# Kernel optimization log

Hardware: AMD Instinct MI355X
Metric: run time of the kernel (lower is better)

## Reference

```python
import jax, jax.numpy as jnp
import numpy as np

B, NH, NPTS = 16, 64, 2048
NEIGHS = 20   # knn neighbors in EdgeConv
K_SEL = 512   # topk points selected
EPS = 1e-5    # BatchNorm eps


def setup_inputs() -> dict:
    key = jax.random.key(0)
    ks = jax.random.split(key, 8)
    xyz = jax.random.normal(ks[0], (B, 3, NPTS), jnp.float32)
    seq1 = jax.random.normal(ks[1], (B, NH, NPTS), jnp.float32)
    perm = jax.random.permutation(ks[2], NPTS)
    # fc: Conv1d(n_h,n_h,1) + BN1d (eval-mode stats)
    W_fc = jax.random.normal(ks[3], (NH, NH), jnp.float32) * 0.1
    b_fc = jnp.zeros((NH,), jnp.float32)
    bn1_gamma = jnp.ones((NH,), jnp.float32)
    bn1_beta = jnp.zeros((NH,), jnp.float32)
    bn1_mean = jnp.zeros((NH,), jnp.float32)
    bn1_var = jnp.ones((NH,), jnp.float32)
    # EdgeConv: Conv2d(2*n_h, n_h, 1, bias=False) + BN2d
    W_ec = jax.random.normal(ks[4], (NH, 2 * NH), jnp.float32) * 0.05
    bn2_gamma = jnp.ones((NH,), jnp.float32)
    bn2_beta = jnp.zeros((NH,), jnp.float32)
    bn2_mean = jnp.zeros((NH,), jnp.float32)
    bn2_var = jnp.ones((NH,), jnp.float32)
    # Discriminator Bilinear(n_h, n_h, 1), xavier-uniform weight, zero bias
    lim = float(np.sqrt(6.0 / (NH + NH)))
    W_b = jax.random.uniform(ks[5], (NH, NH), jnp.float32, -lim, lim)
    b_b = jnp.zeros((), jnp.float32)
    return dict(xyz=xyz, seq1=seq1, perm=perm, W_fc=W_fc, b_fc=b_fc,
                bn1_gamma=bn1_gamma, bn1_beta=bn1_beta, bn1_mean=bn1_mean, bn1_var=bn1_var,
                W_ec=W_ec, bn2_gamma=bn2_gamma, bn2_beta=bn2_beta, bn2_mean=bn2_mean, bn2_var=bn2_var,
                W_b=W_b, b_b=b_b)


def reference(xyz, seq1, perm, W_fc, b_fc, bn1_gamma, bn1_beta, bn1_mean, bn1_var,
              W_ec, bn2_gamma, bn2_beta, bn2_mean, bn2_var, W_b, b_b):
    def fc(x):  # x: [B, NH, N] -> Conv1d(1x1) + BN1d(eval) + ReLU
        y = jnp.einsum('oc,bcn->bon', W_fc, x) + b_fc[None, :, None]
        scale = bn1_gamma / jnp.sqrt(bn1_var + EPS)
        y = (y - bn1_mean[None, :, None]) * scale[None, :, None] + bn1_beta[None, :, None]
        return jax.nn.relu(y)

    seq2 = seq1[:, :, perm]                       # shuffled negative sample
    h1 = fc(seq1)                                 # [B, NH, N]
    h2 = fc(seq2)

    # --- EdgeConv(center): knn in feature space ---
    x2 = jnp.sum(h1 * h1, axis=1)                 # [B, N]
    d = 2.0 * jnp.einsum('bcn,bcm->bnm', h1, h1) - x2[:, :, None] - x2[:, None, :]
    _, nidx = jax.lax.top_k(d, NEIGHS)            # [B, N, K] nearest neighbors

    pts = jnp.transpose(h1, (0, 2, 1))            # [B, N, NH]
    nb = jax.vmap(lambda p, i: p[i])(pts, nidx)   # [B, N, K, NH] gather
    ctr = jnp.broadcast_to(pts[:, :, None, :], nb.shape)
    feat = jnp.concatenate([nb - ctr, ctr], axis=-1)   # [B, N, K, 2*NH]

    y = jnp.einsum('bnkc,oc->bnko', feat, W_ec)   # 1x1 conv
    scale2 = bn2_gamma / jnp.sqrt(bn2_var + EPS)
    y = (y - bn2_mean) * scale2 + bn2_beta        # BN2d over channel (last axis)
    y = jnp.where(y >= 0, y, 0.2 * y)             # LeakyReLU(0.2)
    hn1 = jnp.max(y, axis=2)                      # max over k -> [B, N, NH]

    X = jax.nn.sigmoid(hn1)                       # summary per point, [B, N, NH]

    # --- Discriminator: Bilinear(n_h, n_h, 1) ---
    h1t = pts                                     # [B, N, NH]
    h2t = jnp.transpose(h2, (0, 2, 1))
    sc1 = jnp.einsum('bnc,cd,bnd->bn', h1t, W_b, X) + b_b
    sc2 = jnp.einsum('bnc,cd,bnd->bn', h2t, W_b, X) + b_b
    ret = jnp.concatenate([sc1, sc2], axis=1)     # [B, 2N]

    scores = jax.nn.sigmoid(sc1)                  # ret[:, :N]
    values, idx = jax.lax.top_k(scores, K_SEL)    # [B, K_SEL]

    gi = idx[:, None, :]
    seq_static = jnp.take_along_axis(seq1, jnp.broadcast_to(gi, (B, NH, K_SEL)), axis=2)
    seq = seq_static * values[:, None, :]
    xyz_static = jnp.take_along_axis(xyz, jnp.broadcast_to(gi, (B, 3, K_SEL)), axis=2)
    xyz_out = xyz_static * values[:, None, :]
    return seq, values, idx, ret, xyz_static, xyz_out
```

## Files before the change

kernel.cpp:

```cpp
#include <hip/hip_runtime.h>
#include <math.h>

#define NB 16
#define NH 64
#define NPTS 2048
#define NEIGHS 20
#define KSEL 512
#define EPSV 1e-5f
#define NINF -3.0e38f

#define OFF_SEQ 0
#define OFF_VAL (NB*NH*KSEL)
#define OFF_IDX (OFF_VAL + NB*KSEL)
#define OFF_RET (OFF_IDX + NB*KSEL)
#define OFF_XST (OFF_RET + NB*2*NPTS)
#define OFF_XO  (OFF_XST + NB*3*KSEL)

__device__ __forceinline__ bool better(float av, int ai, float bv, int bi) {
  return (av > bv) || (av == bv && ai < bi);
}

__global__ __launch_bounds__(256) void k_fc(const float* __restrict__ seq1,
                                            const float* __restrict__ Wfc,
                                            const float* __restrict__ bfc,
                                            const float* __restrict__ b1g,
                                            const float* __restrict__ b1b,
                                            const float* __restrict__ b1m,
                                            const float* __restrict__ b1v,
                                            const float* __restrict__ Wec,
                                            float* __restrict__ pts,
                                            float* __restrict__ ptsT,
                                            float* __restrict__ G1,
                                            float* __restrict__ G2,
                                            float* __restrict__ x2) {
  const int b = blockIdx.y, n0 = blockIdx.x * 64;
  const int tid = threadIdx.x, l = tid & 63, w = tid >> 6;
  const int n = n0 + l;
  __shared__ float ptL[64*65];
  const float* sq = seq1 + (size_t)b*NH*NPTS + n;
  float x[64];
  #pragma unroll
  for (int c = 0; c < 64; ++c) x[c] = sq[(size_t)c*NPTS];

  for (int oo = 0; oo < 16; ++oo) {
    const int o = w*16 + oo;
    float acc = 0.f;
    const float* ar = Wfc + o*64;
    #pragma unroll
    for (int c = 0; c < 64; c += 4) {
      float4 a4 = *(const float4*)(ar + c);
      acc = fmaf(a4.x, x[c],   acc);
      acc = fmaf(a4.y, x[c+1], acc);
      acc = fmaf(a4.z, x[c+2], acc);
      acc = fmaf(a4.w, x[c+3], acc);
    }
    float s1 = b1g[o] / sqrtf(b1v[o] + EPSV);
    float y  = (acc + bfc[o] - b1m[o]) * s1 + b1b[o];
    ptL[l*65 + o] = fmaxf(y, 0.f);
  }
  __syncthreads();
  float pt[64];
  #pragma unroll
  for (int c = 0; c < 64; ++c) pt[c] = ptL[l*65 + c];
  if (w == 0) {
    float s2 = 0.f;
    #pragma unroll
    for (int c = 0; c < 64; ++c) s2 = fmaf(pt[c], pt[c], s2);
    x2[(size_t)b*NPTS + n] = s2;
  }
  const size_t base = ((size_t)b*NPTS + n0)*NH;
  for (int t = w*16; t < w*16 + 16; ++t) pts[base + t*64 + l] = ptL[t*65 + l];
  for (int c = w*16; c < w*16 + 16; ++c)
    ptsT[((size_t)b*NH + c)*NPTS + n] = ptL[l*65 + c];
  __syncthreads();

  for (int oo = 0; oo < 16; ++oo) {
    const int o = w*16 + oo;
    const float* w1 = Wec + o*128;
    float a1 = 0.f;
    #pragma unroll
    for (int c = 0; c < 64; c += 4) {
      float4 u = *(const float4*)(w1 + c);
      a1 = fmaf(u.x, pt[c],   a1); a1 = fmaf(u.y, pt[c+1], a1);
      a1 = fmaf(u.z, pt[c+2], a1); a1 = fmaf(u.w, pt[c+3], a1);
    }
    ptL[l*65 + o] = a1;
  }
  __syncthreads();
  for (int t = w*16; t < w*16 + 16; ++t) G1[base + t*64 + l] = ptL[t*65 + l];
  __syncthreads();

  for (int oo = 0; oo < 16; ++oo) {
    const int o = w*16 + oo;
    const float* w2 = Wec + o*128 + 64;
    float a2 = 0.f;
    #pragma unroll
    for (int c = 0; c < 64; c += 4) {
      float4 v = *(const float4*)(w2 + c);
      a2 = fmaf(v.x, pt[c],   a2); a2 = fmaf(v.y, pt[c+1], a2);
      a2 = fmaf(v.z, pt[c+2], a2); a2 = fmaf(v.w, pt[c+3], a2);
    }
    ptL[l*65 + o] = a2;
  }
  __syncthreads();
  for (int t = w*16; t < w*16 + 16; ++t) G2[base + t*64 + l] = ptL[t*65 + l];
}

#define FMA4(A, s, F) { (A).x = fmaf((s),(F).x,(A).x); (A).y = fmaf((s),(F).y,(A).y); \
                        (A).z = fmaf((s),(F).z,(A).z); (A).w = fmaf((s),(F).w,(A).w); }

#define CAND(KV, CI) { float cv_=(KV); int ci_=(CI); \
  { bool c_=cv_>L0v; float nv_=c_?cv_:L0v; int ni_=c_?ci_:L0i; float ov_=L0v; int oi_=L0i; cv_=c_?ov_:cv_; ci_=c_?oi_:ci_; L0v=nv_; L0i=ni_; } \
  { bool c_=cv_>L1v; float nv_=c_?cv_:L1v; int ni_=c_?ci_:L1i; float ov_=L1v; int oi_=L1i; cv_=c_?ov_:cv_; ci_=c_?oi_:ci_; L1v=nv_; L1i=ni_; } \
  { bool c_=cv_>L2v; float nv_=c_?cv_:L2v; int ni_=c_?ci_:L2i; float ov_=L2v; int oi_=L2i; cv_=c_?ov_:cv_; ci_=c_?oi_:ci_; L2v=nv_; L2i=ni_; } \
  { bool c_=cv_>L3v; float nv_=c_?cv_:L3v; int ni_=c_?ci_:L3i; float ov_=L3v; int oi_=L3i; cv_=c_?ov_:cv_; ci_=c_?oi_:ci_; L3v=nv_; L3i=ni_; } \
  bool bb_=better(cv_,ci_,bv,bi); bv=bb_?cv_:bv; bi=bb_?ci_:bi; }

#define FCAND(JB, AV, XV) { bool av_=((taken_>>(JB))&1u)==0u; float kv_=fmaf(2.f,(AV),-(XV)); \
  int ci_=cbase+((JB)>>2)*256+((JB)&3); bool bt_=av_&&better(kv_,ci_,pv,pi); \
  pv=bt_?kv_:pv; pi=bt_?ci_:pi; pj=bt_?(JB):pj; }

#define SELROW(T0,T1,T2,T3,RI) { \
  float L0v=NINF,L1v=NINF,L2v=NINF,L3v=NINF; \
  int   L0i=0x7fffffff,L1i=0x7fffffff,L2i=0x7fffffff,L3i=0x7fffffff; \
  float bv=NINF; int bi=0x7fffffff; \
  CAND(fmaf(2.f,(T0).x,-x0.x), cbase+0)   CAND(fmaf(2.f,(T0).y,-x0.y), cbase+1) \
  CAND(fmaf(2.f,(T0).z,-x0.z), cbase+2)   CAND(fmaf(2.f,(T0).w,-x0.w), cbase+3) \
  CAND(fmaf(2.f,(T1).x,-x1.x), cbase+256) CAND(fmaf(2.f,(T1).y,-x1.y), cbase+257) \
  CAND(fmaf(2.f,(T1).z,-x1.z), cbase+258) CAND(fmaf(2.f,(T1).w,-x1.w), cbase+259) \
  CAND(fmaf(2.f,(T2).x,-x2q.x), cbase+512) CAND(fmaf(2.f,(T2).y,-x2q.y), cbase+513) \
  CAND(fmaf(2.f,(T2).z,-x2q.z), cbase+514) CAND(fmaf(2.f,(T2).w,-x2q.w), cbase+515) \
  CAND(fmaf(2.f,(T3).x,-x3.x), cbase+768) CAND(fmaf(2.f,(T3).y,-x3.y), cbase+769) \
  CAND(fmaf(2.f,(T3).z,-x3.z), cbase+770) CAND(fmaf(2.f,(T3).w,-x3.w), cbase+771) \
  float h0v=L0v,h1v=L1v,h2v=L2v,h3v=L3v; \
  int   e0_=L0i,e1_=L1i,e2_=L2i,e3_=L3i; \
  float myV_=0.f; int myNb_=0; float lastv_=NINF; int lasti_=0x7fffffff; \
  for (int t20_=0; t20_<NEIGHS; ++t20_) { \
    float gv=h0v; int gi=e0_; \
    for (int m_=32; m_>=1; m_>>=1) { \
      float ov=__shfl_xor(gv,m_,64); int oi=__shfl_xor(gi,m_,64); \
      bool bt=better(ov,oi,gv,gi); gv=bt?ov:gv; gi=bt?oi:gi; } \
    bool win=(h0v==gv)&&(e0_==gi); \
    h0v=win?h1v:h0v; e0_=win?e1_:e0_; h1v=win?h2v:h1v; e1_=win?e2_:e1_; \
    h2v=win?h3v:h2v; e2_=win?e3_:e2_; h3v=win?NINF:h3v; e3_=win?0x7fffffff:e3_; \
    if (l==t20_){myV_=gv;myNb_=gi;} lastv_=gv; lasti_=gi; \
  } \
  bool flag_ = better(bv, bi, lastv_, lasti_); \
  if (__any((int)flag_)) { \
    unsigned taken_ = 0u; \
    for (int t20_=0; t20_<NEIGHS; ++t20_) { \
      float pv=NINF; int pi=0x7fffffff; int pj=0; \
      FCAND(0,(T0).x,x0.x)  FCAND(1,(T0).y,x0.y)  FCAND(2,(T0).z,x0.z)  FCAND(3,(T0).w,x0.w) \
      FCAND(4,(T1).x,x1.x)  FCAND(5,(T1).y,x1.y)  FCAND(6,(T1).z,x1.z)  FCAND(7,(T1).w,x1.w) \
      FCAND(8,(T2).x,x2q.x) FCAND(9,(T2).y,x2q.y) FCAND(10,(T2).z,x2q.z) FCAND(11,(T2).w,x2q.w) \
      FCAND(12,(T3).x,x3.x) FCAND(13,(T3).y,x3.y) FCAND(14,(T3).z,x3.z) FCAND(15,(T3).w,x3.w) \
      float gv=pv; int gi=pi; \
      for (int m_=32; m_>=1; m_>>=1) { \
        float ov=__shfl_xor(gv,m_,64); int oi=__shfl_xor(gi,m_,64); \
        bool bt=better(ov,oi,gv,gi); gv=bt?ov:gv; gi=bt?oi:gi; } \
      if ((pv==gv)&&(pi==gi)) taken_ |= (1u<<pj); \
      if (l==t20_){myV_=gv;myNb_=gi;} \
    } \
  } \
  if (l < NEIGHS) { \
    mrgV[((g*4+(RI))*2+h)*20 + l] = myV_; \
    mrgI[((g*4+(RI))*2+h)*20 + l] = myNb_; \
  } }

__global__ __launch_bounds__(512, 2) void k_knn(const float* __restrict__ pts,
                                                const float* __restrict__ ptsT,
                                                const float* __restrict__ x2,
                                                int* __restrict__ nidx) {
  const int lin = blockIdx.x;
  const int b  = ((lin & 7) << 1) | ((lin >> 3) & 1);
  const int rg = lin >> 4;
  const int tid = threadIdx.x, w = tid >> 6, l = tid & 63;
  const int g = w >> 1, h = w & 1;
  const int r0 = rg*16;

  __shared__ float colB[2][8192];
  __shared__ float rowS[16*64];
  __shared__ float mrgV[16*2*20];
  __shared__ int   mrgI[16*2*20];

  const float* Tb = ptsT + (size_t)b*NH*NPTS;

  if (tid < 256) {
    int rr = tid >> 4, c4 = (tid & 15) * 4;
    *(float4*)&rowS[rr*64 + c4] =
        *(const float4*)(pts + ((size_t)b*NPTS + r0 + rr)*NH + c4);
  }
  #pragma unroll
  for (int s = 0; s < 4; ++s) {
    float4 v = *(const float4*)(Tb + (w*4+s)*256 + l*4);
    *(float4*)&colB[0][(w*4+s)*256 + l*4] = v;
  }
  __syncthreads();

  float4 A00={0,0,0,0},A01={0,0,0,0},A02={0,0,0,0},A03={0,0,0,0};
  float4 A10={0,0,0,0},A11={0,0,0,0},A12={0,0,0,0},A13={0,0,0,0};
  float4 A20={0,0,0,0},A21={0,0,0,0},A22={0,0,0,0},A23={0,0,0,0};
  float4 A30={0,0,0,0},A31={0,0,0,0},A32={0,0,0,0},A33={0,0,0,0};

  #pragma unroll 1
  for (int t = 0; t < 16; ++t) {
    float4 st0, st1, st2, st3;
    if (t < 15) {
      const float* src = Tb + (size_t)(t+1)*8192 + w*1024 + l*4;
      st0 = *(const float4*)(src);
      st1 = *(const float4*)(src + 256);
      st2 = *(const float4*)(src + 512);
      st3 = *(const float4*)(src + 768);
    }
    const float* cb = &colB[t & 1][h*1024 + l*4];
    const float* rs = &rowS[(g*4)*64 + t*4];
    #pragma unroll
    for (int k = 0; k < 4; ++k) {
      float4 f0 = *(const float4*)(cb + k*2048);
      float4 f1 = *(const float4*)(cb + k*2048 + 256);
      float4 f2 = *(const float4*)(cb + k*2048 + 512);
      float4 f3 = *(const float4*)(cb + k*2048 + 768);
      float r0k = rs[k], r1k = rs[64 + k], r2k = rs[128 + k], r3k = rs[192 + k];
      FMA4(A00,r0k,f0) FMA4(A01,r0k,f1) FMA4(A02,r0k,f2) FMA4(A03,r0k,f3)
      FMA4(A10,r1k,f0) FMA4(A11,r1k,f1) FMA4(A12,r1k,f2) FMA4(A13,r1k,f3)
      FMA4(A20,r2k,f0) FMA4(A21,r2k,f1) FMA4(A22,r2k,f2) FMA4(A23,r2k,f3)
      FMA4(A30,r3k,f0) FMA4(A31,r3k,f1) FMA4(A32,r3k,f2) FMA4(A33,r3k,f3)
    }
    if (t < 15) {
      float* d = &colB[(t+1)&1][w*1024 + l*4];
      *(float4*)(d)       = st0;
      *(float4*)(d + 256) = st1;
      *(float4*)(d + 512) = st2;
      *(float4*)(d + 768) = st3;
    }
    __syncthreads();
  }

  const int cbase = h*1024 + l*4;
  const float* x2b = x2 + (size_t)b*NPTS + cbase;
  float4 x0  = *(const float4*)(x2b);
  float4 x1  = *(const float4*)(x2b + 256);
  float4 x2q = *(const float4*)(x2b + 512);
  float4 x3  = *(const float4*)(x2b + 768);

  SELROW(A00,A01,A02,A03,0)
  SELROW(A10,A11,A12,A13,1)
  SELROW(A20,A21,A22,A23,2)
  SELROW(A30,A31,A32,A33,3)

  __syncthreads();
  if (w == 0 && l < 16) {
    const float* va = &mrgV[(l*2+0)*20]; const int* ja = &mrgI[(l*2+0)*20];
    const float* vb = &mrgV[(l*2+1)*20]; const int* jb = &mrgI[(l*2+1)*20];
    int* dst = nidx + ((size_t)b*NPTS + r0 + l)*NEIGHS;
    int ia = 0, ib = 0;
    #pragma unroll 1
    for (int k = 0; k < NEIGHS; ++k) {
      float av = va[ia]; int ai = ja[ia];
      float bv2 = vb[ib]; int bi2 = jb[ib];
      bool ta = better(av, ai, bv2, bi2);
      dst[k] = ta ? ai : bi2;
      ia += ta ? 1 : 0; ib += ta ? 0 : 1;
    }
  }
}

__global__ __launch_bounds__(256) void k_score(const float* __restrict__ pts,
    const float* __restrict__ G1, const float* __restrict__ G2,
    const int* __restrict__ nidx, const int* __restrict__ perm,
    const float* __restrict__ Wb,
    const float* __restrict__ b2g, const float* __restrict__ b2b,
    const float* __restrict__ b2m, const float* __restrict__ b2v,
    const float* __restrict__ bb,
    float* __restrict__ sc1w, float* __restrict__ out) {
  const int b = blockIdx.y;
  const int n0 = blockIdx.x * 16;
  const int tid = threadIdx.x, l = tid & 63, w = tid >> 6;
  __shared__ float WbS[64*65];
  for (int i = tid; i < 64*64; i += 256) WbS[(i >> 6)*65 + (i & 63)] = Wb[i];
  __syncthreads();
  const float sc2v = b2g[l] / sqrtf(b2v[l] + EPSV);
  const float mean2 = b2m[l], beta2 = b2b[l];
  const float bbv = bb[0];
  const float* G1b = G1 + (size_t)b*NPTS*NH;
  for (int it = 0; it < 4; ++it) {
    const int n = n0 + it*4 + w;
    const size_t ro = (size_t)b*NPTS*NH + (size_t)n*NH;
    const float base = G2[ro + l] - G1[ro + l];
    const int* nb = nidx + ((size_t)b*NPTS + n)*NEIGHS;
    float mx = NINF;
    #pragma unroll
    for (int k = 0; k < NEIGHS; ++k) {
      int m = nb[k];
      float val = G1b[(size_t)m*NH + l] + base;
      float y = (val - mean2) * sc2v + beta2;
      y = (y >= 0.f) ? y : 0.2f*y;
      mx = fmaxf(mx, y);
    }
    float X = 1.f / (1.f + expf(-mx));
    double v = 0.0;
    #pragma unroll
    for (int d = 0; d < 64; ++d) {
      float xd = __shfl(X, d, 64);
      v += (double)WbS[l*65 + d] * (double)xd;
    }
    float p1 = pts[ro + l];
    int pn = perm[n];
    float p2 = pts[(size_t)b*NPTS*NH + (size_t)pn*NH + l];
    double s1 = (double)p1 * v;
    double s2 = (double)p2 * v;
    #pragma unroll
    for (int off = 32; off > 0; off >>= 1) {
      s1 += __shfl_xor(s1, off, 64);
      s2 += __shfl_xor(s2, off, 64);
    }
    if (l == 0) {
      float r1 = (float)(s1 + (double)bbv);
      float r2 = (float)(s2 + (double)bbv);
      sc1w[(size_t)b*NPTS + n] = r1;
      out[OFF_RET + (size_t)b*2*NPTS + n] = r1;
      out[OFF_RET + (size_t)b*2*NPTS + NPTS + n] = r2;
    }
  }
}

__global__ __launch_bounds__(256) void k_select(const float* __restrict__ sc1w,
    const float* __restrict__ seq1, const float* __restrict__ xyz,
    float* __restrict__ out) {
  const int b = blockIdx.x, tid = threadIdx.x;
  __shared__ unsigned long long keys[NPTS];
  __shared__ float valS[KSEL];
  __shared__ int idxS[KSEL];
  for (int i = tid; i < NPTS; i += 256) {
    float f = sc1w[(size_t)b*NPTS + i];
    unsigned u = __float_as_uint(f);
    u = (u & 0x80000000u) ? ~u : (u | 0x80000000u);
    keys[i] = ((unsigned long long)(~u) << 32) | (unsigned)i;
  }
  __syncthreads();
  for (int k = 2; k <= NPTS; k <<= 1) {
    for (int j = k >> 1; j > 0; j >>= 1) {
      for (int i = tid; i < NPTS; i += 256) {
        int l2 = i ^ j;
        if (l2 > i) {
          unsigned long long a = keys[i], c = keys[l2];
          bool up = ((i & k) == 0);
          if ((a > c) == up) { keys[i] = c; keys[l2] = a; }
        }
      }
      __syncthreads();
    }
  }
  for (int i = tid; i < KSEL; i += 256) {
    unsigned long long key = keys[i];
    int sidx = (int)(key & 0xffffffffULL);
    unsigned u = ~(unsigned)(key >> 32);
    unsigned fb = (u & 0x80000000u) ? (u & 0x7fffffffu) : ~u;
    float f = __uint_as_float(fb);
    float val = 1.f / (1.f + expf(-f));
    valS[i] = val; idxS[i] = sidx;
    out[OFF_VAL + (size_t)b*KSEL + i] = val;
    out[OFF_IDX + (size_t)b*KSEL + i] = (float)sidx;
  }
  __syncthreads();
  for (int t = tid; t < NH*KSEL; t += 256) {
    int c = t >> 9, i = t & (KSEL-1);
    float sv = seq1[((size_t)b*NH + c)*NPTS + idxS[i]];
    out[OFF_SEQ + (((size_t)b*NH + c) << 9) + i] = sv * valS[i];
  }
  for (int t = tid; t < 3*KSEL; t += 256) {
    int c = t >> 9, i = t & (KSEL-1);
    float xv = xyz[((size_t)b*3 + c)*NPTS + idxS[i]];
    out[OFF_XST + (((size_t)b*3 + c) << 9) + i] = xv;
    out[OFF_XO  + (((size_t)b*3 + c) << 9) + i] = xv * valS[i];
  }
}

extern "C" void kernel_launch(void* const* d_in, const int* in_sizes, int n_in,
                              void* d_out, int out_size, void* d_ws, size_t ws_size,
                              hipStream_t stream) {
  const float* xyz  = (const float*)d_in[0];
  const float* seq1 = (const float*)d_in[1];
  const int*   perm = (const int*)d_in[2];
  const float* Wfc  = (const float*)d_in[3];
  const float* bfc  = (const float*)d_in[4];
  const float* b1g  = (const float*)d_in[5];
  const float* b1b  = (const float*)d_in[6];
  const float* b1m  = (const float*)d_in[7];
  const float* b1v  = (const float*)d_in[8];
  const float* Wec  = (const float*)d_in[9];
  const float* b2g  = (const float*)d_in[10];
  const float* b2b  = (const float*)d_in[11];
  const float* b2m  = (const float*)d_in[12];
  const float* b2v  = (const float*)d_in[13];
  const float* Wb   = (const float*)d_in[14];
  const float* bb   = (const float*)d_in[15];
  float* out = (float*)d_out;

  float* ws   = (float*)d_ws;
  float* pts  = ws;
  float* ptsT = pts + (size_t)NB*NPTS*NH;
  float* G1   = ptsT + (size_t)NB*NPTS*NH;
  float* G2   = G1  + (size_t)NB*NPTS*NH;
  float* x2   = G2  + (size_t)NB*NPTS*NH;
  float* sc1w = x2  + (size_t)NB*NPTS;
  int*   nidx = (int*)(sc1w + (size_t)NB*NPTS);

  hipLaunchKernelGGL(k_fc, dim3(NPTS/64, NB), dim3(256), 0, stream,
                     seq1, Wfc, bfc, b1g, b1b, b1m, b1v, Wec, pts, ptsT, G1, G2, x2);
  hipLaunchKernelGGL(k_knn, dim3(NB*NPTS/16), dim3(512), 0, stream,
                     pts, ptsT, x2, nidx);
  hipLaunchKernelGGL(k_score, dim3(NPTS/16, NB), dim3(256), 0, stream,
                     pts, G1, G2, nidx, perm, Wb, b2g, b2b, b2m, b2v, bb, sc1w, out);
  hipLaunchKernelGGL(k_select, dim3(NB), dim3(256), 0, stream,
                     sc1w, seq1, xyz, out);
}
```

Before: 783.7 us.

## Replace wave-shuffle kNN top-20 selection with packed-key shared-memory merge and fallback

Each lane now keeps a per-lane top-4 of packed 64-bit keys (order-preserving float bits plus inverted index). These keys are dumped to shared memory, which reuses the column buffers. Two lanes per wave then serially merge the 512 candidates per row into a top-20 insertion list. If any lane's 4th-best could still belong in the top 20, a full-row recompute and a single-thread scan over all 2048 columns serves as the exact fallback. This removes the 20-round shuffle reductions per row, but the merge is heavily serialized and the fallback path is very slow. The occupancy hint also drops from 2 blocks to the default.

```diff
diff --git a/kernel.cpp b/kernel.cpp
--- a/kernel.cpp
+++ b/kernel.cpp
@@ -9,6 +9,8 @@
 #define EPSV 1e-5f
 #define NINF -3.0e38f
 
+typedef unsigned long long ull;
+
 #define OFF_SEQ 0
 #define OFF_VAL (NB*NH*KSEL)
 #define OFF_IDX (OFF_VAL + NB*KSEL)
@@ -18,6 +20,12 @@
 
 __device__ __forceinline__ bool better(float av, int ai, float bv, int bi) {
   return (av > bv) || (av == bv && ai < bi);
+}
+
+__device__ __forceinline__ ull packkey(float v, int ci) {
+  unsigned u = __float_as_uint(v);
+  u = (u & 0x80000000u) ? ~u : (u | 0x80000000u);
+  return ((ull)u << 32) | (unsigned)(~ci);
 }
 
 __global__ __launch_bounds__(256) void k_fc(const float* __restrict__ seq1,
@@ -109,68 +117,36 @@
 #define FMA4(A, s, F) { (A).x = fmaf((s),(F).x,(A).x); (A).y = fmaf((s),(F).y,(A).y); \
                         (A).z = fmaf((s),(F).z,(A).z); (A).w = fmaf((s),(F).w,(A).w); }
 
-#define CAND(KV, CI) { float cv_=(KV); int ci_=(CI); \
-  { bool c_=cv_>L0v; float nv_=c_?cv_:L0v; int ni_=c_?ci_:L0i; float ov_=L0v; int oi_=L0i; cv_=c_?ov_:cv_; ci_=c_?oi_:ci_; L0v=nv_; L0i=ni_; } \
-  { bool c_=cv_>L1v; float nv_=c_?cv_:L1v; int ni_=c_?ci_:L1i; float ov_=L1v; int oi_=L1i; cv_=c_?ov_:cv_; ci_=c_?oi_:ci_; L1v=nv_; L1i=ni_; } \
-  { bool c_=cv_>L2v; float nv_=c_?cv_:L2v; int ni_=c_?ci_:L2i; float ov_=L2v; int oi_=L2i; cv_=c_?ov_:cv_; ci_=c_?oi_:ci_; L2v=nv_; L2i=ni_; } \
-  { bool c_=cv_>L3v; float nv_=c_?cv_:L3v; int ni_=c_?ci_:L3i; float ov_=L3v; int oi_=L3i; cv_=c_?ov_:cv_; ci_=c_?oi_:ci_; L3v=nv_; L3i=ni_; } \
-  bool bb_=better(cv_,ci_,bv,bi); bv=bb_?cv_:bv; bi=bb_?ci_:bi; }
-
-#define FCAND(JB, AV, XV) { bool av_=((taken_>>(JB))&1u)==0u; float kv_=fmaf(2.f,(AV),-(XV)); \
-  int ci_=cbase+((JB)>>2)*256+((JB)&3); bool bt_=av_&&better(kv_,ci_,pv,pi); \
-  pv=bt_?kv_:pv; pi=bt_?ci_:pi; pj=bt_?(JB):pj; }
-
-#define SELROW(T0,T1,T2,T3,RI) { \
-  float L0v=NINF,L1v=NINF,L2v=NINF,L3v=NINF; \
-  int   L0i=0x7fffffff,L1i=0x7fffffff,L2i=0x7fffffff,L3i=0x7fffffff; \
-  float bv=NINF; int bi=0x7fffffff; \
-  CAND(fmaf(2.f,(T0).x,-x0.x), cbase+0)   CAND(fmaf(2.f,(T0).y,-x0.y), cbase+1) \
-  CAND(fmaf(2.f,(T0).z,-x0.z), cbase+2)   CAND(fmaf(2.f,(T0).w,-x0.w), cbase+3) \
-  CAND(fmaf(2.f,(T1).x,-x1.x), cbase+256) CAND(fmaf(2.f,(T1).y,-x1.y), cbase+257) \
-  CAND(fmaf(2.f,(T1).z,-x1.z), cbase+258) CAND(fmaf(2.f,(T1).w,-x1.w), cbase+259) \
-  CAND(fmaf(2.f,(T2).x,-x2q.x), cbase+512) CAND(fmaf(2.f,(T2).y,-x2q.y), cbase+513) \
-  CAND(fmaf(2.f,(T2).z,-x2q.z), cbase+514) CAND(fmaf(2.f,(T2).w,-x2q.w), cbase+515) \
-  CAND(fmaf(2.f,(T3).x,-x3.x), cbase+768) CAND(fmaf(2.f,(T3).y,-x3.y), cbase+769) \
-  CAND(fmaf(2.f,(T3).z,-x3.z), cbase+770) CAND(fmaf(2.f,(T3).w,-x3.w), cbase+771) \
-  float h0v=L0v,h1v=L1v,h2v=L2v,h3v=L3v; \
-  int   e0_=L0i,e1_=L1i,e2_=L2i,e3_=L3i; \
-  float myV_=0.f; int myNb_=0; float lastv_=NINF; int lasti_=0x7fffffff; \
-  for (int t20_=0; t20_<NEIGHS; ++t20_) { \
-    float gv=h0v; int gi=e0_; \
-    for (int m_=32; m_>=1; m_>>=1) { \
-      float ov=__shfl_xor(gv,m_,64); int oi=__shfl_xor(gi,m_,64); \
-      bool bt=better(ov,oi,gv,gi); gv=bt?ov:gv; gi=bt?oi:gi; } \
-    bool win=(h0v==gv)&&(e0_==gi); \
-    h0v=win?h1v:h0v; e0_=win?e1_:e0_; h1v=win?h2v:h1v; e1_=win?e2_:e1_; \
-    h2v=win?h3v:h2v; e2_=win?e3_:e2_; h3v=win?NINF:h3v; e3_=win?0x7fffffff:e3_; \
-    if (l==t20_){myV_=gv;myNb_=gi;} lastv_=gv; lasti_=gi; \
-  } \
-  bool flag_ = better(bv, bi, lastv_, lasti_); \
-  if (__any((int)flag_)) { \
-    unsigned taken_ = 0u; \
-    for (int t20_=0; t20_<NEIGHS; ++t20_) { \
-      float pv=NINF; int pi=0x7fffffff; int pj=0; \
-      FCAND(0,(T0).x,x0.x)  FCAND(1,(T0).y,x0.y)  FCAND(2,(T0).z,x0.z)  FCAND(3,(T0).w,x0.w) \
-      FCAND(4,(T1).x,x1.x)  FCAND(5,(T1).y,x1.y)  FCAND(6,(T1).z,x1.z)  FCAND(7,(T1).w,x1.w) \
-      FCAND(8,(T2).x,x2q.x) FCAND(9,(T2).y,x2q.y) FCAND(10,(T2).z,x2q.z) FCAND(11,(T2).w,x2q.w) \
-      FCAND(12,(T3).x,x3.x) FCAND(13,(T3).y,x3.y) FCAND(14,(T3).z,x3.z) FCAND(15,(T3).w,x3.w) \
-      float gv=pv; int gi=pi; \
-      for (int m_=32; m_>=1; m_>>=1) { \
-        float ov=__shfl_xor(gv,m_,64); int oi=__shfl_xor(gi,m_,64); \
-        bool bt=better(ov,oi,gv,gi); gv=bt?ov:gv; gi=bt?oi:gi; } \
-      if ((pv==gv)&&(pi==gi)) taken_ |= (1u<<pj); \
-      if (l==t20_){myV_=gv;myNb_=gi;} \
-    } \
-  } \
-  if (l < NEIGHS) { \
-    mrgV[((g*4+(RI))*2+h)*20 + l] = myV_; \
-    mrgI[((g*4+(RI))*2+h)*20 + l] = myNb_; \
-  } }
-
-__global__ __launch_bounds__(512, 2) void k_knn(const float* __restrict__ pts,
-                                                const float* __restrict__ ptsT,
-                                                const float* __restrict__ x2,
-                                                int* __restrict__ nidx) {
+#define INS4(CAND) { ull c_=(CAND); \
+  { bool b_=c_>K0; ull n_=b_?c_:K0; ull o_=K0; c_=b_?o_:c_; K0=n_; } \
+  { bool b_=c_>K1; ull n_=b_?c_:K1; ull o_=K1; c_=b_?o_:c_; K1=n_; } \
+  { bool b_=c_>K2; ull n_=b_?c_:K2; ull o_=K2; c_=b_?o_:c_; K2=n_; } \
+  { bool b_=c_>K3; ull n_=b_?c_:K3; c_=0;       K3=n_; } }
+
+#define BUILDROW(T0,T1,T2,T3,RI) { \
+  ull K0=0,K1=0,K2=0,K3=0; \
+  INS4(packkey(fmaf(2.f,(T0).x,-x0.x), cbase+0))   INS4(packkey(fmaf(2.f,(T0).y,-x0.y), cbase+1)) \
+  INS4(packkey(fmaf(2.f,(T0).z,-x0.z), cbase+2))   INS4(packkey(fmaf(2.f,(T0).w,-x0.w), cbase+3)) \
+  INS4(packkey(fmaf(2.f,(T1).x,-x1.x), cbase+256)) INS4(packkey(fmaf(2.f,(T1).y,-x1.y), cbase+257)) \
+  INS4(packkey(fmaf(2.f,(T1).z,-x1.z), cbase+258)) INS4(packkey(fmaf(2.f,(T1).w,-x1.w), cbase+259)) \
+  INS4(packkey(fmaf(2.f,(T2).x,-x2q.x), cbase+512)) INS4(packkey(fmaf(2.f,(T2).y,-x2q.y), cbase+513)) \
+  INS4(packkey(fmaf(2.f,(T2).z,-x2q.z), cbase+514)) INS4(packkey(fmaf(2.f,(T2).w,-x2q.w), cbase+515)) \
+  INS4(packkey(fmaf(2.f,(T3).x,-x3.x), cbase+768)) INS4(packkey(fmaf(2.f,(T3).y,-x3.y), cbase+769)) \
+  INS4(packkey(fmaf(2.f,(T3).z,-x3.z), cbase+770)) INS4(packkey(fmaf(2.f,(T3).w,-x3.w), cbase+771)) \
+  { int row_ = g*4+(RI), cell_ = h*64+l; \
+    dumpS[(0*16+row_)*128 + cell_] = K0; \
+    dumpS[(1*16+row_)*128 + cell_] = K1; \
+    dumpS[(2*16+row_)*128 + cell_] = K2; \
+    dumpS[(3*16+row_)*128 + cell_] = K3; } }
+
+#define INS20U(CAND) { ull c_=(CAND); \
+  _Pragma("unroll") \
+  for (int k_=0; k_<20; ++k_) { bool b_=c_>L[k_]; ull n_=b_?c_:L[k_]; ull o_=L[k_]; c_=b_?o_:c_; L[k_]=n_; } }
+
+__global__ __launch_bounds__(512) void k_knn(const float* __restrict__ pts,
+                                             const float* __restrict__ ptsT,
+                                             const float* __restrict__ x2,
+                                             int* __restrict__ nidx) {
   const int lin = blockIdx.x;
   const int b  = ((lin & 7) << 1) | ((lin >> 3) & 1);
   const int rg = lin >> 4;
@@ -178,10 +154,13 @@
   const int g = w >> 1, h = w & 1;
   const int r0 = rg*16;
 
-  __shared__ float colB[2][8192];
-  __shared__ float rowS[16*64];
-  __shared__ float mrgV[16*2*20];
-  __shared__ int   mrgI[16*2*20];
+  __shared__ __align__(16) unsigned char smem[65536 + 4096 + 64];
+  float* colB0 = (float*)smem;
+  float* colB1 = (float*)(smem + 32768);
+  ull*   dumpS = (ull*)smem;
+  ull*   kbuf  = (ull*)smem;
+  float* rowS  = (float*)(smem + 65536);
+  int*   flagS = (int*)(smem + 65536 + 4096);
 
   const float* Tb = ptsT + (size_t)b*NH*NPTS;
 
@@ -193,7 +172,7 @@
   #pragma unroll
   for (int s = 0; s < 4; ++s) {
     float4 v = *(const float4*)(Tb + (w*4+s)*256 + l*4);
-    *(float4*)&colB[0][(w*4+s)*256 + l*4] = v;
+    *(float4*)&colB0[(w*4+s)*256 + l*4] = v;
   }
   __syncthreads();
 
@@ -212,7 +191,7 @@
       st2 = *(const float4*)(src + 512);
       st3 = *(const float4*)(src + 768);
     }
-    const float* cb = &colB[t & 1][h*1024 + l*4];
+    const float* cb = ((t & 1) ? colB1 : colB0) + h*1024 + l*4;
     const float* rs = &rowS[(g*4)*64 + t*4];
     #pragma unroll
     for (int k = 0; k < 4; ++k) {
@@ -227,7 +206,7 @@
       FMA4(A30,r3k,f0) FMA4(A31,r3k,f1) FMA4(A32,r3k,f2) FMA4(A33,r3k,f3)
     }
     if (t < 15) {
-      float* d = &colB[(t+1)&1][w*1024 + l*4];
+      float* d = ((t & 1) ? colB0 : colB1) + w*1024 + l*4;
       *(float4*)(d)       = st0;
       *(float4*)(d + 256) = st1;
       *(float4*)(d + 512) = st2;
@@ -243,24 +222,69 @@
   float4 x2q = *(const float4*)(x2b + 512);
   float4 x3  = *(const float4*)(x2b + 768);
 
-  SELROW(A00,A01,A02,A03,0)
-  SELROW(A10,A11,A12,A13,1)
-  SELROW(A20,A21,A22,A23,2)
-  SELROW(A30,A31,A32,A33,3)
-
-  __syncthreads();
-  if (w == 0 && l < 16) {
-    const float* va = &mrgV[(l*2+0)*20]; const int* ja = &mrgI[(l*2+0)*20];
-    const float* vb = &mrgV[(l*2+1)*20]; const int* jb = &mrgI[(l*2+1)*20];
-    int* dst = nidx + ((size_t)b*NPTS + r0 + l)*NEIGHS;
-    int ia = 0, ib = 0;
+  BUILDROW(A00,A01,A02,A03,0)
+  BUILDROW(A10,A11,A12,A13,1)
+  BUILDROW(A20,A21,A22,A23,2)
+  BUILDROW(A30,A31,A32,A33,3)
+  __syncthreads();
+
+  if (l < 2) {
+    const int row = w*2 + l;
+    ull L[20];
+    #pragma unroll
+    for (int k = 0; k < 20; ++k) L[k] = 0;
+    ull maxB = 0;
     #pragma unroll 1
-    for (int k = 0; k < NEIGHS; ++k) {
-      float av = va[ia]; int ai = ja[ia];
-      float bv2 = vb[ib]; int bi2 = jb[ib];
-      bool ta = better(av, ai, bv2, bi2);
-      dst[k] = ta ? ai : bi2;
-      ia += ta ? 1 : 0; ib += ta ? 0 : 1;
+    for (int cell = 0; cell < 128; ++cell) {
+      int cs = (l*64 + cell) & 127;
+      ull e0 = dumpS[(0*16+row)*128 + cs];
+      ull e1 = dumpS[(1*16+row)*128 + cs];
+      ull e2 = dumpS[(2*16+row)*128 + cs];
+      ull e3 = dumpS[(3*16+row)*128 + cs];
+      maxB = (e3 > maxB) ? e3 : maxB;
+      if (e0 > L[19]) { INS20U(e0) }
+      if (e1 > L[19]) { INS20U(e1) }
+      if (e2 > L[19]) { INS20U(e2) }
+      if (e3 > L[19]) { INS20U(e3) }
+    }
+    bool bad = (maxB > L[19]);
+    flagS[row] = bad ? 1 : 0;
+    if (!bad) {
+      int* dst = nidx + ((size_t)b*NPTS + r0 + row)*NEIGHS;
+      #pragma unroll
+      for (int k = 0; k < 20; ++k) dst[k] = (int)(~(unsigned)(L[k] & 0xffffffffULL)) & 0x7fffffff;
+    }
+  }
+  __syncthreads();
+
+  #pragma unroll 1
+  for (int r = 0; r < 16; ++r) {
+    if (flagS[r]) {
+      #pragma unroll 1
+      for (int col = tid; col < NPTS; col += 512) {
+        float acc = 0.f;
+        const float* Tc = Tb + col;
+        #pragma unroll
+        for (int c = 0; c < 64; ++c)
+          acc = fmaf(rowS[r*64 + c], Tc[(size_t)c*NPTS], acc);
+        float key = fmaf(2.f, acc, -x2[(size_t)b*NPTS + col]);
+        kbuf[col] = packkey(key, col);
+      }
+      __syncthreads();
+      if (tid == 0) {
+        ull L[20];
+        #pragma unroll
+        for (int k = 0; k < 20; ++k) L[k] = 0;
+        #pragma unroll 1
+        for (int col = 0; col < NPTS; ++col) {
+          ull e = kbuf[col];
+          if (e > L[19]) { INS20U(e) }
+        }
+        int* dst = nidx + ((size_t)b*NPTS + r0 + r)*NEIGHS;
+        #pragma unroll
+        for (int k = 0; k < 20; ++k) dst[k] = (int)(~(unsigned)(L[k] & 0xffffffffULL)) & 0x7fffffff;
+      }
+      __syncthreads();
     }
   }
 }
```

Result: slower. 3.059 ms (+290.3%).
